# Kernel optimization log

Measured on AMD Instinct MI355X. Metric: run time of the kernel, lower is better.

## Reference

```python
import jax, jax.numpy as jnp
import numpy as np

QUERY_DIM = 1024
CONTEXT_DIM = 1024
HEADS = 8
DIM_HEAD = 64
INNER = HEADS * DIM_HEAD  # 512
SCALE = DIM_HEAD ** -0.5


def setup_inputs() -> dict:
    key = jax.random.key(0)
    ks = jax.random.split(key, 7)
    B, N, M = 2, 2048, 2048
    x = jax.random.normal(ks[0], (B, N, QUERY_DIM), dtype=jnp.float32)
    context = jax.random.normal(ks[1], (B, M, CONTEXT_DIM), dtype=jnp.float32)
    # nn.Linear weights (stored as [out, in] in torch; we use [in, out] here)
    Wq = jax.random.normal(ks[2], (QUERY_DIM, INNER), dtype=jnp.float32) * (QUERY_DIM ** -0.5)
    Wk = jax.random.normal(ks[3], (CONTEXT_DIM, INNER), dtype=jnp.float32) * (CONTEXT_DIM ** -0.5)
    Wv = jax.random.normal(ks[4], (CONTEXT_DIM, INNER), dtype=jnp.float32) * (CONTEXT_DIM ** -0.5)
    Wo = jax.random.normal(ks[5], (INNER, QUERY_DIM), dtype=jnp.float32) * (INNER ** -0.5)
    bo = jax.random.normal(ks[6], (QUERY_DIM,), dtype=jnp.float32) * 0.01
    return {"x": x, "context": context, "Wq": Wq, "Wk": Wk, "Wv": Wv, "Wo": Wo, "bo": bo}


def reference(x, context, Wq, Wk, Wv, Wo, bo):
    B, N, _ = x.shape
    M = context.shape[1]
    # projections (no bias, matching nn.Linear(bias=False))
    q = (x @ Wq).reshape(B, N, HEADS, DIM_HEAD)          # b i h d
    k = (context @ Wk).reshape(B, M, HEADS, DIM_HEAD)    # b j h d
    v = (context @ Wv).reshape(B, M, HEADS, DIM_HEAD)    # b j h d
    # scores in fp32 (ATTN_PRECISION=='fp32' path)
    sim = jnp.einsum('bihd,bjhd->bhij', q.astype(jnp.float32), k.astype(jnp.float32)) * SCALE
    attn = jax.nn.softmax(sim, axis=-1).astype(v.dtype)  # b h i j
    out = jnp.einsum('bhij,bjhd->bihd', attn, v).reshape(B, N, INNER)
    return out @ Wo + bo  # dropout p=0.0 is identity
```

## Files before the change

### kernel.cpp

```cpp
#include <hip/hip_runtime.h>
#include <math.h>

typedef __bf16 bf16_t;
typedef __bf16 bf16x8 __attribute__((ext_vector_type(8)));
typedef __bf16 bf16x4 __attribute__((ext_vector_type(4)));
typedef float  f32x4  __attribute__((ext_vector_type(4)));

#define MFMA16(a, b, c) __builtin_amdgcn_mfma_f32_16x16x32_bf16((a), (b), (c), 0, 0, 0)

#define INNER   512
#define DHEAD   64
#define QSCALE  0.18033688f

__device__ __forceinline__ void g2l(const bf16_t* g, bf16_t* l) {
  __builtin_amdgcn_global_load_lds(
      (const __attribute__((address_space(1))) unsigned int*)g,
      (__attribute__((address_space(3))) unsigned int*)l, 16, 0, 0);
}

__global__ __launch_bounds__(256) void pre_w_k(const float* __restrict__ Wq,
                                               const float* __restrict__ Wk,
                                               const float* __restrict__ Wv,
                                               const float* __restrict__ Wo,
                                               bf16_t* __restrict__ WqT,
                                               bf16_t* __restrict__ WkT,
                                               bf16_t* __restrict__ WvT,
                                               bf16_t* __restrict__ WoT) {
  __shared__ float tile[64][65];
  int t = blockIdx.x;
  int z = t >> 7, bid = t & 127;
  const float* W; bf16_t* WT; int K, N;
  if (z == 0)      { W = Wq; WT = WqT; K = 1024; N = 512; }
  else if (z == 1) { W = Wk; WT = WkT; K = 1024; N = 512; }
  else if (z == 2) { W = Wv; WT = WvT; K = 1024; N = 512; }
  else             { W = Wo; WT = WoT; K = 512;  N = 1024; }
  int tK = K >> 6;
  int kt = bid % tK, nt = bid / tK;
  int k0 = kt << 6, n0 = nt << 6;
  for (int idx = threadIdx.x; idx < 4096; idx += 256) {
    int r = idx >> 6, c = idx & 63;
    tile[r][c] = W[(size_t)(k0 + r) * N + n0 + c];
  }
  __syncthreads();
  for (int idx = threadIdx.x; idx < 4096; idx += 256) {
    int r = idx >> 6, c = idx & 63;
    WT[(size_t)(n0 + r) * K + k0 + c] = (bf16_t)tile[c][r];
  }
}

template<int BM, bool AF32>
__device__ __forceinline__ void gemm_core(const void* __restrict__ Ap,
                                          const bf16_t* __restrict__ Bt,
                                          int K, int N, int row0, int n0,
                                          int mode, float scale,
                                          bf16_t* __restrict__ Cb,
                                          float* __restrict__ Cf,
                                          const float* __restrict__ bias) {
  constexpr int MI = BM / 32;
  __shared__ bf16_t As[2 * BM * 64];
  __shared__ bf16_t Bs[2 * 128 * 64];
  const int tid = threadIdx.x;
  const int w = tid >> 6, lane = tid & 63, quad = lane >> 4, l16 = lane & 15;

  const int sr8  = lane >> 3;
  const int slog = ((lane & 7) ^ sr8) << 3;
  const float*  gaF = nullptr;
  const bf16_t* gaB = nullptr;
  {
    size_t aoff = (size_t)(row0 + w * (BM / 4) + sr8) * K + slog;
    if constexpr (AF32) gaF = (const float*)Ap + aoff;
    else                gaB = (const bf16_t*)Ap + aoff;
  }
  const bf16_t* gb = Bt + (size_t)(n0 + w * 32 + sr8) * K + slog;
  bf16_t* lA = As + w * (BM / 4) * 64;
  bf16_t* lB = Bs + w * 2048;

  f32x4 acc[MI][4];
#pragma unroll
  for (int i = 0; i < MI; ++i)
#pragma unroll
    for (int j = 0; j < 4; ++j) acc[i][j] = f32x4{0.f, 0.f, 0.f, 0.f};

  const int mrow = (w & 1) * (BM / 2), ncol = (w >> 1) << 6;
  const int KT = K >> 6;

  if constexpr (AF32) {
#pragma unroll
    for (int p = 0; p < MI; ++p) {
      const float* s = gaF + (size_t)(p * 8) * K;
      f32x4 f0 = *(const f32x4*)s;
      f32x4 f1 = *(const f32x4*)(s + 4);
      bf16x8 h;
#pragma unroll
      for (int e = 0; e < 4; ++e) { h[e] = (bf16_t)f0[e]; h[4 + e] = (bf16_t)f1[e]; }
      *(bf16x8*)&lA[p * 512 + lane * 8] = h;
    }
  } else {
#pragma unroll
    for (int p = 0; p < MI; ++p)
      g2l(gaB + (size_t)(p * 8) * K, lA + p * 512);
  }
#pragma unroll
  for (int p = 0; p < 4; ++p)
    g2l(gb + (size_t)(p * 8) * K, lB + p * 512);

  for (int kc = 0; kc < KT; ++kc) {
    const int curA = (kc & 1) * (BM * 64), nxtA = ((kc + 1) & 1) * (BM * 64);
    const int curB = (kc & 1) * 8192,      nxtB = ((kc + 1) & 1) * 8192;
    __syncthreads();
    f32x4 fpre[2 * MI];
    const bool pf = (kc + 1 < KT);
    if (pf) {
      const int k0 = (kc + 1) * 64;
#pragma unroll
      for (int p = 0; p < 4; ++p)
        g2l(gb + (size_t)(p * 8) * K + k0, lB + nxtB + p * 512);
      if constexpr (AF32) {
#pragma unroll
        for (int p = 0; p < MI; ++p) {
          const float* s = gaF + (size_t)(p * 8) * K + k0;
          fpre[2 * p]     = *(const f32x4*)s;
          fpre[2 * p + 1] = *(const f32x4*)(s + 4);
        }
      } else {
#pragma unroll
        for (int p = 0; p < MI; ++p)
          g2l(gaB + (size_t)(p * 8) * K + k0, lA + nxtA + p * 512);
      }
    }
#pragma unroll
    for (int ks = 0; ks < 2; ++ks) {
      const int phys = ((ks * 4 + quad) ^ (l16 & 7)) << 3;
      bf16x8 af[MI], bfr[4];
#pragma unroll
      for (int i = 0; i < MI; ++i)
        af[i] = *(const bf16x8*)&As[curA + (mrow + i * 16 + l16) * 64 + phys];
#pragma unroll
      for (int j = 0; j < 4; ++j)
        bfr[j] = *(const bf16x8*)&Bs[curB + (ncol + j * 16 + l16) * 64 + phys];
#pragma unroll
      for (int i = 0; i < MI; ++i)
#pragma unroll
        for (int j = 0; j < 4; ++j)
          acc[i][j] = MFMA16(af[i], bfr[j], acc[i][j]);
    }
    if (pf) {
      if constexpr (AF32) {
#pragma unroll
        for (int p = 0; p < MI; ++p) {
          bf16x8 h;
#pragma unroll
          for (int e = 0; e < 4; ++e) {
            h[e]     = (bf16_t)fpre[2 * p][e];
            h[4 + e] = (bf16_t)fpre[2 * p + 1][e];
          }
          *(bf16x8*)&lA[nxtA + p * 512 + lane * 8] = h;
        }
      }
    }
  }

#pragma unroll
  for (int i = 0; i < MI; ++i) {
    int row = row0 + mrow + i * 16 + quad * 4;
#pragma unroll
    for (int j = 0; j < 4; ++j) {
      int col = n0 + ncol + j * 16 + l16;
      if (mode == 2) {
        int bb = row >> 11, key = row & 2047;
        int hh = col >> 6,  d   = col & 63;
        bf16x4 v = { (bf16_t)acc[i][j][0], (bf16_t)acc[i][j][1],
                     (bf16_t)acc[i][j][2], (bf16_t)acc[i][j][3] };
        *(bf16x4*)&Cb[((size_t)((bb * 8 + hh) * 64 + d)) * 2048 + key] = v;
      } else {
#pragma unroll
        for (int r = 0; r < 4; ++r) {
          if (mode == 1) Cf[(size_t)(row + r) * N + col] = acc[i][j][r] + bias[col];
          else           Cb[(size_t)(row + r) * N + col] = (bf16_t)(acc[i][j][r] * scale);
        }
      }
    }
  }
}

__global__ __launch_bounds__(256, 2) void gemm_qkv_k(const float* __restrict__ x,
                                                     const float* __restrict__ ctx,
                                                     const bf16_t* __restrict__ WqT,
                                                     const bf16_t* __restrict__ WkT,
                                                     const bf16_t* __restrict__ WvT,
                                                     bf16_t* __restrict__ Qb,
                                                     bf16_t* __restrict__ Kb,
                                                     bf16_t* __restrict__ Vt) {
  int bid = blockIdx.x;
  int z = bid >> 7;
  int xcd  = bid & 7;
  int slot = (bid & 127) >> 3;
  int m = (xcd << 2) | (slot >> 2);
  int n = slot & 3;
  const float* A   = (z == 0) ? x   : ctx;
  const bf16_t* Bt = (z == 0) ? WqT : (z == 1) ? WkT : WvT;
  bf16_t* C        = (z == 0) ? Qb  : (z == 1) ? Kb  : Vt;
  int mode         = (z == 2) ? 2 : 0;
  float scale      = (z == 0) ? QSCALE : 1.0f;
  gemm_core<128, true>(A, Bt, 1024, 512, m * 128, n * 128, mode, scale,
                       C, nullptr, nullptr);
}

__global__ __launch_bounds__(256, 2) void gemm_out_k(const bf16_t* __restrict__ AO,
                                                     const bf16_t* __restrict__ WoT,
                                                     const float* __restrict__ bo,
                                                     float* __restrict__ out) {
  int bid = blockIdx.x;
  int xcd  = bid & 7;
  int slot = bid >> 3;
  int m = (xcd << 3) | (slot >> 3);
  int n = slot & 7;
  gemm_core<64, false>(AO, WoT, 512, 1024, m * 64, n * 128,
                       1, 1.0f, nullptr, out, bo);
}

__global__ __launch_bounds__(256, 2) void attn_k(const bf16_t* __restrict__ Qb,
                                                 const bf16_t* __restrict__ Kb,
                                                 const bf16_t* __restrict__ Vt,
                                                 bf16_t* __restrict__ AO) {
  const int tid = threadIdx.x;
  const int w = tid >> 6, lane = tid & 63, quad = lane >> 4, l16 = lane & 15;
  int bid = blockIdx.x;
  int xcd  = bid & 7;
  int slot = bid >> 3;
  const int qt = slot & 31;
  const int bh = (xcd << 1) | (slot >> 5);
  const int b = bh >> 3, h = bh & 7;

  __shared__ bf16_t Ks[2 * 128 * 64];
  __shared__ bf16_t Vs[64 * 128];
  __shared__ bf16_t Ps[64 * 136];

  const int qrow = b * 2048 + qt * 64 + w * 16 + l16;
  const bf16_t* qptr = Qb + (size_t)qrow * INNER + h * DHEAD;
  bf16x8 bq[2];
  bq[0] = *(const bf16x8*)(qptr + quad * 8);
  bq[1] = *(const bf16x8*)(qptr + 32 + quad * 8);

  f32x4 o[4];
#pragma unroll
  for (int dt = 0; dt < 4; ++dt) o[dt] = f32x4{0.f, 0.f, 0.f, 0.f};
  float m_s = -__builtin_inff(), l_s = 0.f;

  const bf16_t* kbase  = Kb + ((size_t)b * 2048) * INNER + h * DHEAD;
  const bf16_t* vtbase = Vt + ((size_t)bh * 64) * 2048;

  const int krow = lane >> 3;
  const int kcol = ((lane & 7) ^ (lane >> 3)) << 3;
  const int vrow = lane >> 4;

#pragma unroll
  for (int p = 0; p < 4; ++p)
    g2l(kbase + (size_t)(w * 32 + p * 8 + krow) * INNER + kcol,
        &Ks[w * 2048 + p * 512]);

  for (int kt = 0; kt < 16; ++kt) {
    const int cur = (kt & 1) * 8192, nxt = ((kt + 1) & 1) * 8192;
    __syncthreads();
    if (kt < 16 - 1) {
#pragma unroll
      for (int p = 0; p < 4; ++p)
        g2l(kbase + (size_t)((kt + 1) * 128 + w * 32 + p * 8 + krow) * INNER + kcol,
            &Ks[nxt + w * 2048 + p * 512]);
    }
#pragma unroll
    for (int p = 0; p < 4; ++p) {
      int vlog = ((lane & 15) ^ ((p * 4 + vrow) & 15)) << 3;
      g2l(vtbase + (size_t)(w * 16 + p * 4 + vrow) * 2048 + kt * 128 + vlog,
          &Vs[w * 2048 + p * 512]);
    }

    f32x4 s[8];
#pragma unroll
    for (int jt = 0; jt < 8; ++jt) s[jt] = f32x4{0.f, 0.f, 0.f, 0.f};
#pragma unroll
    for (int jt = 0; jt < 8; ++jt) {
#pragma unroll
      for (int ks = 0; ks < 2; ++ks) {
        int phys = ((ks * 4 + quad) ^ (l16 & 7)) << 3;
        bf16x8 ak = *(const bf16x8*)&Ks[cur + (jt * 16 + l16) * 64 + phys];
        s[jt] = MFMA16(ak, bq[ks], s[jt]);
      }
    }

    float mx = -__builtin_inff();
#pragma unroll
    for (int jt = 0; jt < 8; ++jt) {
      float a = fmaxf(fmaxf(s[jt][0], s[jt][1]), fmaxf(s[jt][2], s[jt][3]));
      mx = fmaxf(mx, a);
    }
    mx = fmaxf(mx, __shfl_xor(mx, 16, 64));
    mx = fmaxf(mx, __shfl_xor(mx, 32, 64));
    float mnew = fmaxf(m_s, mx);
    float alpha = __builtin_amdgcn_exp2f(m_s - mnew);
    float rs = 0.f;
#pragma unroll
    for (int jt = 0; jt < 8; ++jt) {
#pragma unroll
      for (int r = 0; r < 4; ++r) {
        float p = __builtin_amdgcn_exp2f(s[jt][r] - mnew);
        s[jt][r] = p;
        rs += p;
      }
    }
    rs += __shfl_xor(rs, 16, 64);
    rs += __shfl_xor(rs, 32, 64);
    l_s = l_s * alpha + rs;
    m_s = mnew;
#pragma unroll
    for (int dt = 0; dt < 4; ++dt) o[dt] *= alpha;

#pragma unroll
    for (int jt = 0; jt < 8; ++jt) {
      bf16x4 pk = { (bf16_t)s[jt][0], (bf16_t)s[jt][1],
                    (bf16_t)s[jt][2], (bf16_t)s[jt][3] };
      *(bf16x4*)&Ps[(w * 16 + l16) * 136 + jt * 16 + quad * 4] = pk;
    }

    __syncthreads();

#pragma unroll
    for (int kc = 0; kc < 4; ++kc) {
      bf16x8 bp = *(const bf16x8*)&Ps[(w * 16 + l16) * 136 + kc * 32 + quad * 8];
#pragma unroll
      for (int dt = 0; dt < 4; ++dt) {
        int phys = ((kc * 4 + quad) ^ l16) << 3;
        bf16x8 av = *(const bf16x8*)&Vs[(dt * 16 + l16) * 128 + phys];
        o[dt] = MFMA16(av, bp, o[dt]);
      }
    }
  }

  float inv = 1.0f / l_s;
#pragma unroll
  for (int dt = 0; dt < 4; ++dt) {
    bf16x4 ov = { (bf16_t)(o[dt][0] * inv), (bf16_t)(o[dt][1] * inv),
                  (bf16_t)(o[dt][2] * inv), (bf16_t)(o[dt][3] * inv) };
    *(bf16x4*)&Ps[(w * 16 + l16) * 136 + dt * 16 + quad * 4] = ov;
  }
  __syncthreads();
  {
    int sr = tid >> 2, sc = (tid & 3) << 4;
    int4 r0 = *(const int4*)&Ps[sr * 136 + sc];
    int4 r1 = *(const int4*)&Ps[sr * 136 + sc + 8];
    bf16_t* aout = AO + ((size_t)(b * 2048 + qt * 64 + sr)) * INNER + h * DHEAD + sc;
    *(int4*)aout       = r0;
    *(int4*)(aout + 8) = r1;
  }
}

extern "C" void kernel_launch(void* const* d_in, const int* in_sizes, int n_in,
                              void* d_out, int out_size, void* d_ws, size_t ws_size,
                              hipStream_t stream) {
  const float* x   = (const float*)d_in[0];
  const float* ctx = (const float*)d_in[1];
  const float* Wq  = (const float*)d_in[2];
  const float* Wk  = (const float*)d_in[3];
  const float* Wv  = (const float*)d_in[4];
  const float* Wo  = (const float*)d_in[5];
  const float* bo  = (const float*)d_in[6];
  float* out = (float*)d_out;

  char* ws = (char*)d_ws;
  const size_t MB = 1048576;
  bf16_t* WqT = (bf16_t*)(ws + 0 * MB);
  bf16_t* WkT = (bf16_t*)(ws + 1 * MB);
  bf16_t* WvT = (bf16_t*)(ws + 2 * MB);
  bf16_t* WoT = (bf16_t*)(ws + 3 * MB);
  bf16_t* Qb  = (bf16_t*)(ws + 4 * MB);
  bf16_t* Kb  = (bf16_t*)(ws + 8 * MB);
  bf16_t* Vt  = (bf16_t*)(ws + 12 * MB);
  bf16_t* AO  = (bf16_t*)(ws + 16 * MB);

  pre_w_k<<<512, 256, 0, stream>>>(Wq, Wk, Wv, Wo, WqT, WkT, WvT, WoT);
  gemm_qkv_k<<<384, 256, 0, stream>>>(x, ctx, WqT, WkT, WvT, Qb, Kb, Vt);
  attn_k<<<512, 256, 0, stream>>>(Qb, Kb, Vt, AO);
  gemm_out_k<<<512, 256, 0, stream>>>(AO, WoT, bo, out);
}
```

Baseline: 166.7 us.

## Deepen QKV GEMM prefetch pipeline with manual waitcnt and add MFMA priority in attention

Splits the fp32-input QKV GEMM into its own core. It prefetches the fp32 A tile two k-steps ahead in ping-pong registers and unrolls the k loop by two. Explicit s_waitcnt vmcnt counts replace the generic __syncthreads, so global loads stay in flight across the MFMA work. The attention kernel also raises wave priority around its MFMA blocks with s_setprio, to favour matrix issue over other waves. The cost is more register pressure and hand-tuned wait counts that can break if the load counts change; the wrapped k0a index also makes the last steps issue redundant loads.

Measured after the change: 162.2 us. 2.7% less time.

```diff
diff --git a/kernel.cpp b/kernel.cpp
--- a/kernel.cpp
+++ b/kernel.cpp
@@ -48,120 +48,109 @@
   }
 }
 
-template<int BM, bool AF32>
-__device__ __forceinline__ void gemm_core(const void* __restrict__ Ap,
-                                          const bf16_t* __restrict__ Bt,
-                                          int K, int N, int row0, int n0,
-                                          int mode, float scale,
-                                          bf16_t* __restrict__ Cb,
-                                          float* __restrict__ Cf,
-                                          const float* __restrict__ bias) {
-  constexpr int MI = BM / 32;
-  __shared__ bf16_t As[2 * BM * 64];
+#define QKV_STEP(kc, CUR, NXT, PRC, PRF)                                         \
+  {                                                                              \
+    asm volatile("s_waitcnt vmcnt(8) lgkmcnt(0)" ::: "memory");                  \
+    __builtin_amdgcn_s_barrier();                                                \
+    __builtin_amdgcn_sched_barrier(0);                                           \
+    {                                                                            \
+      const int k0b = (((kc) + 1) & (KT - 1)) * 64;                              \
+      _Pragma("unroll")                                                          \
+      for (int p = 0; p < 4; ++p)                                                \
+        g2l(gb + (size_t)(p * 8) * K + k0b, lB + (NXT) + p * 512);               \
+    }                                                                            \
+    {                                                                            \
+      const int k0a = (((kc) + 2) & (KT - 1)) * 64;                              \
+      _Pragma("unroll")                                                          \
+      for (int p = 0; p < 4; ++p) {                                              \
+        const float* s_ = ga + (size_t)(p * 8) * K + k0a;                        \
+        PRF[2 * p]     = *(const f32x4*)s_;                                      \
+        PRF[2 * p + 1] = *(const f32x4*)(s_ + 4);                                \
+      }                                                                          \
+    }                                                                            \
+    _Pragma("unroll")                                                            \
+    for (int ks = 0; ks < 2; ++ks) {                                             \
+      const int phys = ((ks * 4 + quad) ^ (l16 & 7)) << 3;                       \
+      bf16x8 af[4], bfr[4];                                                      \
+      _Pragma("unroll")                                                          \
+      for (int i = 0; i < 4; ++i)                                                \
+        af[i] = *(const bf16x8*)&As[(CUR) + (mrow + i * 16 + l16) * 64 + phys];  \
+      _Pragma("unroll")                                                          \
+      for (int j = 0; j < 4; ++j)                                                \
+        bfr[j] = *(const bf16x8*)&Bs[(CUR) + (ncol + j * 16 + l16) * 64 + phys]; \
+      _Pragma("unroll")                                                          \
+      for (int i = 0; i < 4; ++i)                                                \
+        _Pragma("unroll")                                                        \
+        for (int j = 0; j < 4; ++j)                                              \
+          acc[i][j] = MFMA16(af[i], bfr[j], acc[i][j]);                          \
+    }                                                                            \
+    asm volatile("s_waitcnt vmcnt(12)" ::: "memory");                            \
+    __builtin_amdgcn_sched_barrier(0);                                           \
+    _Pragma("unroll")                                                            \
+    for (int p = 0; p < 4; ++p) {                                                \
+      bf16x8 h_;                                                                 \
+      _Pragma("unroll")                                                          \
+      for (int e = 0; e < 4; ++e) {                                              \
+        h_[e]     = (bf16_t)PRC[2 * p][e];                                       \
+        h_[4 + e] = (bf16_t)PRC[2 * p + 1][e];                                   \
+      }                                                                          \
+      *(bf16x8*)&lA[(NXT) + p * 512 + lane * 8] = h_;                            \
+    }                                                                            \
+  }
+
+__device__ __forceinline__ void gemm_qkv_core(const float* __restrict__ A,
+                                              const bf16_t* __restrict__ Bt,
+                                              int row0, int n0,
+                                              int mode, float scale,
+                                              bf16_t* __restrict__ Cb) {
+  constexpr int K = 1024, KT = 16;
+  __shared__ bf16_t As[2 * 128 * 64];
   __shared__ bf16_t Bs[2 * 128 * 64];
   const int tid = threadIdx.x;
   const int w = tid >> 6, lane = tid & 63, quad = lane >> 4, l16 = lane & 15;
-
   const int sr8  = lane >> 3;
   const int slog = ((lane & 7) ^ sr8) << 3;
-  const float*  gaF = nullptr;
-  const bf16_t* gaB = nullptr;
-  {
-    size_t aoff = (size_t)(row0 + w * (BM / 4) + sr8) * K + slog;
-    if constexpr (AF32) gaF = (const float*)Ap + aoff;
-    else                gaB = (const bf16_t*)Ap + aoff;
-  }
-  const bf16_t* gb = Bt + (size_t)(n0 + w * 32 + sr8) * K + slog;
-  bf16_t* lA = As + w * (BM / 4) * 64;
+  const float*  ga = A  + (size_t)(row0 + w * 32 + sr8) * K + slog;
+  const bf16_t* gb = Bt + (size_t)(n0   + w * 32 + sr8) * K + slog;
+  bf16_t* lA = As + w * 2048;
   bf16_t* lB = Bs + w * 2048;
 
-  f32x4 acc[MI][4];
-#pragma unroll
-  for (int i = 0; i < MI; ++i)
+  f32x4 acc[4][4];
+#pragma unroll
+  for (int i = 0; i < 4; ++i)
 #pragma unroll
     for (int j = 0; j < 4; ++j) acc[i][j] = f32x4{0.f, 0.f, 0.f, 0.f};
 
-  const int mrow = (w & 1) * (BM / 2), ncol = (w >> 1) << 6;
-  const int KT = K >> 6;
-
-  if constexpr (AF32) {
-#pragma unroll
-    for (int p = 0; p < MI; ++p) {
-      const float* s = gaF + (size_t)(p * 8) * K;
-      f32x4 f0 = *(const f32x4*)s;
-      f32x4 f1 = *(const f32x4*)(s + 4);
-      bf16x8 h;
-#pragma unroll
-      for (int e = 0; e < 4; ++e) { h[e] = (bf16_t)f0[e]; h[4 + e] = (bf16_t)f1[e]; }
-      *(bf16x8*)&lA[p * 512 + lane * 8] = h;
-    }
-  } else {
-#pragma unroll
-    for (int p = 0; p < MI; ++p)
-      g2l(gaB + (size_t)(p * 8) * K, lA + p * 512);
+  f32x4 pA0[8], pA1[8];
+  const int mrow = (w & 1) << 6, ncol = (w >> 1) << 6;
+
+#pragma unroll
+  for (int p = 0; p < 4; ++p) {
+    const float* s = ga + (size_t)(p * 8) * K;
+    f32x4 f0 = *(const f32x4*)s;
+    f32x4 f1 = *(const f32x4*)(s + 4);
+    bf16x8 h;
+#pragma unroll
+    for (int e = 0; e < 4; ++e) { h[e] = (bf16_t)f0[e]; h[4 + e] = (bf16_t)f1[e]; }
+    *(bf16x8*)&lA[p * 512 + lane * 8] = h;
   }
 #pragma unroll
   for (int p = 0; p < 4; ++p)
     g2l(gb + (size_t)(p * 8) * K, lB + p * 512);
-
-  for (int kc = 0; kc < KT; ++kc) {
-    const int curA = (kc & 1) * (BM * 64), nxtA = ((kc + 1) & 1) * (BM * 64);
-    const int curB = (kc & 1) * 8192,      nxtB = ((kc + 1) & 1) * 8192;
-    __syncthreads();
-    f32x4 fpre[2 * MI];
-    const bool pf = (kc + 1 < KT);
-    if (pf) {
-      const int k0 = (kc + 1) * 64;
-#pragma unroll
-      for (int p = 0; p < 4; ++p)
-        g2l(gb + (size_t)(p * 8) * K + k0, lB + nxtB + p * 512);
-      if constexpr (AF32) {
-#pragma unroll
-        for (int p = 0; p < MI; ++p) {
-          const float* s = gaF + (size_t)(p * 8) * K + k0;
-          fpre[2 * p]     = *(const f32x4*)s;
-          fpre[2 * p + 1] = *(const f32x4*)(s + 4);
-        }
-      } else {
-#pragma unroll
-        for (int p = 0; p < MI; ++p)
-          g2l(gaB + (size_t)(p * 8) * K + k0, lA + nxtA + p * 512);
-      }
-    }
-#pragma unroll
-    for (int ks = 0; ks < 2; ++ks) {
-      const int phys = ((ks * 4 + quad) ^ (l16 & 7)) << 3;
-      bf16x8 af[MI], bfr[4];
-#pragma unroll
-      for (int i = 0; i < MI; ++i)
-        af[i] = *(const bf16x8*)&As[curA + (mrow + i * 16 + l16) * 64 + phys];
-#pragma unroll
-      for (int j = 0; j < 4; ++j)
-        bfr[j] = *(const bf16x8*)&Bs[curB + (ncol + j * 16 + l16) * 64 + phys];
-#pragma unroll
-      for (int i = 0; i < MI; ++i)
-#pragma unroll
-        for (int j = 0; j < 4; ++j)
-          acc[i][j] = MFMA16(af[i], bfr[j], acc[i][j]);
-    }
-    if (pf) {
-      if constexpr (AF32) {
-#pragma unroll
-        for (int p = 0; p < MI; ++p) {
-          bf16x8 h;
-#pragma unroll
-          for (int e = 0; e < 4; ++e) {
-            h[e]     = (bf16_t)fpre[2 * p][e];
-            h[4 + e] = (bf16_t)fpre[2 * p + 1][e];
-          }
-          *(bf16x8*)&lA[nxtA + p * 512 + lane * 8] = h;
-        }
-      }
-    }
-  }
-
-#pragma unroll
-  for (int i = 0; i < MI; ++i) {
+#pragma unroll
+  for (int p = 0; p < 4; ++p) {
+    const float* s = ga + (size_t)(p * 8) * K + 64;
+    pA0[2 * p]     = *(const f32x4*)s;
+    pA0[2 * p + 1] = *(const f32x4*)(s + 4);
+  }
+
+  for (int kc = 0; kc < KT; kc += 2) {
+    QKV_STEP(kc,     0,    8192, pA0, pA1);
+    QKV_STEP(kc + 1, 8192, 0,    pA1, pA0);
+  }
+
+#pragma unroll
+  for (int i = 0; i < 4; ++i) {
     int row = row0 + mrow + i * 16 + quad * 4;
 #pragma unroll
     for (int j = 0; j < 4; ++j) {
@@ -174,11 +163,88 @@
         *(bf16x4*)&Cb[((size_t)((bb * 8 + hh) * 64 + d)) * 2048 + key] = v;
       } else {
 #pragma unroll
-        for (int r = 0; r < 4; ++r) {
-          if (mode == 1) Cf[(size_t)(row + r) * N + col] = acc[i][j][r] + bias[col];
-          else           Cb[(size_t)(row + r) * N + col] = (bf16_t)(acc[i][j][r] * scale);
-        }
+        for (int r = 0; r < 4; ++r)
+          Cb[(size_t)(row + r) * 512 + col] = (bf16_t)(acc[i][j][r] * scale);
       }
+    }
+  }
+}
+
+template<int BM>
+__device__ __forceinline__ void gemm_core(const bf16_t* __restrict__ Ab,
+                                          const bf16_t* __restrict__ Bt,
+                                          int K, int N, int row0, int n0,
+                                          float* __restrict__ Cf,
+                                          const float* __restrict__ bias) {
+  constexpr int MI = BM / 32;
+  __shared__ bf16_t As[2 * BM * 64];
+  __shared__ bf16_t Bs[2 * 128 * 64];
+  const int tid = threadIdx.x;
+  const int w = tid >> 6, lane = tid & 63, quad = lane >> 4, l16 = lane & 15;
+
+  const int sr8  = lane >> 3;
+  const int slog = ((lane & 7) ^ sr8) << 3;
+  const bf16_t* ga = Ab + (size_t)(row0 + w * (BM / 4) + sr8) * K + slog;
+  const bf16_t* gb = Bt + (size_t)(n0   + w * 32 + sr8) * K + slog;
+  bf16_t* lA = As + w * (BM / 4) * 64;
+  bf16_t* lB = Bs + w * 2048;
+
+  f32x4 acc[MI][4];
+#pragma unroll
+  for (int i = 0; i < MI; ++i)
+#pragma unroll
+    for (int j = 0; j < 4; ++j) acc[i][j] = f32x4{0.f, 0.f, 0.f, 0.f};
+
+  const int mrow = (w & 1) * (BM / 2), ncol = (w >> 1) << 6;
+  const int KT = K >> 6;
+
+#pragma unroll
+  for (int p = 0; p < MI; ++p)
+    g2l(ga + (size_t)(p * 8) * K, lA + p * 512);
+#pragma unroll
+  for (int p = 0; p < 4; ++p)
+    g2l(gb + (size_t)(p * 8) * K, lB + p * 512);
+
+  for (int kc = 0; kc < KT; ++kc) {
+    const int curA = (kc & 1) * (BM * 64), nxtA = ((kc + 1) & 1) * (BM * 64);
+    const int curB = (kc & 1) * 8192,      nxtB = ((kc + 1) & 1) * 8192;
+    __syncthreads();
+    if (kc + 1 < KT) {
+      const int k0 = (kc + 1) * 64;
+#pragma unroll
+      for (int p = 0; p < MI; ++p)
+        g2l(ga + (size_t)(p * 8) * K + k0, lA + nxtA + p * 512);
+#pragma unroll
+      for (int p = 0; p < 4; ++p)
+        g2l(gb + (size_t)(p * 8) * K + k0, lB + nxtB + p * 512);
+    }
+#pragma unroll
+    for (int ks = 0; ks < 2; ++ks) {
+      const int phys = ((ks * 4 + quad) ^ (l16 & 7)) << 3;
+      bf16x8 af[MI], bfr[4];
+#pragma unroll
+      for (int i = 0; i < MI; ++i)
+        af[i] = *(const bf16x8*)&As[curA + (mrow + i * 16 + l16) * 64 + phys];
+#pragma unroll
+      for (int j = 0; j < 4; ++j)
+        bfr[j] = *(const bf16x8*)&Bs[curB + (ncol + j * 16 + l16) * 64 + phys];
+#pragma unroll
+      for (int i = 0; i < MI; ++i)
+#pragma unroll
+        for (int j = 0; j < 4; ++j)
+          acc[i][j] = MFMA16(af[i], bfr[j], acc[i][j]);
+    }
+  }
+
+#pragma unroll
+  for (int i = 0; i < MI; ++i) {
+    int row = row0 + mrow + i * 16 + quad * 4;
+#pragma unroll
+    for (int j = 0; j < 4; ++j) {
+      int col = n0 + ncol + j * 16 + l16;
+#pragma unroll
+      for (int r = 0; r < 4; ++r)
+        Cf[(size_t)(row + r) * N + col] = acc[i][j][r] + bias[col];
     }
   }
 }
@@ -202,8 +268,7 @@
   bf16_t* C        = (z == 0) ? Qb  : (z == 1) ? Kb  : Vt;
   int mode         = (z == 2) ? 2 : 0;
   float scale      = (z == 0) ? QSCALE : 1.0f;
-  gemm_core<128, true>(A, Bt, 1024, 512, m * 128, n * 128, mode, scale,
-                       C, nullptr, nullptr);
+  gemm_qkv_core(A, Bt, m * 128, n * 128, mode, scale, C);
 }
 
 __global__ __launch_bounds__(256, 2) void gemm_out_k(const bf16_t* __restrict__ AO,
@@ -215,8 +280,7 @@
   int slot = bid >> 3;
   int m = (xcd << 3) | (slot >> 3);
   int n = slot & 7;
-  gemm_core<64, false>(AO, WoT, 512, 1024, m * 64, n * 128,
-                       1, 1.0f, nullptr, out, bo);
+  gemm_core<64>(AO, WoT, 512, 1024, m * 64, n * 128, out, bo);
 }
 
 __global__ __launch_bounds__(256, 2) void attn_k(const bf16_t* __restrict__ Qb,
@@ -278,6 +342,7 @@
     f32x4 s[8];
 #pragma unroll
     for (int jt = 0; jt < 8; ++jt) s[jt] = f32x4{0.f, 0.f, 0.f, 0.f};
+    __builtin_amdgcn_s_setprio(1);
 #pragma unroll
     for (int jt = 0; jt < 8; ++jt) {
 #pragma unroll
@@ -287,6 +352,7 @@
         s[jt] = MFMA16(ak, bq[ks], s[jt]);
       }
     }
+    __builtin_amdgcn_s_setprio(0);
 
     float mx = -__builtin_inff();
 #pragma unroll
@@ -324,6 +390,7 @@
 
     __syncthreads();
 
+    __builtin_amdgcn_s_setprio(1);
 #pragma unroll
     for (int kc = 0; kc < 4; ++kc) {
       bf16x8 bp = *(const bf16x8*)&Ps[(w * 16 + l16) * 136 + kc * 32 + quad * 8];
@@ -334,6 +401,7 @@
         o[dt] = MFMA16(av, bp, o[dt]);
       }
     }
+    __builtin_amdgcn_s_setprio(0);
   }
 
   float inv = 1.0f / l_s;
```
